# Kernel tuning notes

Hardware: AMD Instinct MI355X
Metric: run time of the kernel (lower is better)

## Reference

```python
import jax, jax.numpy as jnp
import numpy as np

N = 100000      # nodes
E = 640000      # total edges across all relations
D_IN = 128
D_OUT = 128
R = 8           # num_rel
B = 4           # num_bases


def setup_inputs() -> dict:
    key = jax.random.key(0)
    ks = jax.random.split(key, 7)
    return {
        "X": jax.random.normal(ks[0], (N, D_IN), dtype=jnp.float32),
        "edge_src": jax.random.randint(ks[1], (E,), 0, N, dtype=jnp.int32),
        "edge_dst": jax.random.randint(ks[2], (E,), 0, N, dtype=jnp.int32),
        "edge_rel": jax.random.randint(ks[3], (E,), 0, R, dtype=jnp.int32),
        "edge_val": jax.random.uniform(ks[4], (E,), dtype=jnp.float32),
        "w_bases": jax.random.normal(ks[5], (B, D_IN, D_OUT), dtype=jnp.float32) * 0.05,
        "w_rel": jax.random.normal(ks[6], (R, B), dtype=jnp.float32) * 0.5,
    }


def reference(X, edge_src, edge_dst, edge_rel, edge_val, w_bases, w_rel):
    # Per-relation SpMM: support_r = A_r @ X, where A_r rows are destinations.
    # Fuse all relations into one gather + one segmented scatter-add.
    msg = X[edge_src] * edge_val[:, None]                      # [E, D_IN]
    seg = edge_rel.astype(jnp.int32) * N + edge_dst            # combined (rel, dst) id
    supports = jax.ops.segment_sum(msg, seg, num_segments=R * N)
    supports = supports.reshape(R, N, D_IN)                    # == concat of per-rel supports
    # Basis-decomposed relation weights: w[r] = sum_b w_rel[r,b] * w_bases[b]
    w = jnp.einsum("rb,bio->rio", w_rel, w_bases)              # [R, D_IN, D_OUT]
    # cat(supports, dim=1) @ w.view(R*D_IN, D_OUT) == sum_r supports_r @ w_r
    out = jnp.einsum("rni,rio->no", supports, w)               # [N, D_OUT]
    return out
```

## Files before the change

### kernel.cpp

```cpp
#include <hip/hip_runtime.h>
#include <stdint.h>

#define D_IN 128
#define D_OUT 128
#define NREL 8
#define NBASE 4

typedef __attribute__((ext_vector_type(8))) short short8;
typedef __attribute__((ext_vector_type(4))) float floatx4;
typedef __attribute__((ext_vector_type(2))) float floatx2;

__device__ __forceinline__ unsigned short f2bf(float f) {
  unsigned int u = __float_as_uint(f);
  u += 0x7fffu + ((u >> 16) & 1u);
  return (unsigned short)(u >> 16);
}
__device__ __forceinline__ unsigned pack2bf(float lo, float hi) {
  return (unsigned)f2bf(lo) | ((unsigned)f2bf(hi) << 16);
}
__device__ __forceinline__ float bflo(unsigned int u) { return __uint_as_float(u << 16); }
__device__ __forceinline__ float bfhi(unsigned int u) { return __uint_as_float(u & 0xffff0000u); }

__global__ void k_prep(const float4* __restrict__ X, ushort4* __restrict__ Xb, int n4,
                       const float* __restrict__ w_bases, unsigned short* __restrict__ W2T,
                       uint4* __restrict__ counts4, int nc4) {
  int i = blockIdx.x * blockDim.x + threadIdx.x;
  if (i < n4) {
    float4 v = X[i];
    ushort4 o;
    o.x = f2bf(v.x); o.y = f2bf(v.y); o.z = f2bf(v.z); o.w = f2bf(v.w);
    Xb[i] = o;
  }
  if (i < 128 * 512) {
    int o = i >> 9, c = i & 511;
    int k = c >> 2, b = c & 3;
    W2T[i] = f2bf(w_bases[(b * D_IN + k) * D_OUT + o]);
  }
  if (i < nc4) counts4[i] = make_uint4(0u, 0u, 0u, 0u);
}

__global__ void k_count(const int* __restrict__ dst, int* __restrict__ counts, int E) {
  int i = blockIdx.x * blockDim.x + threadIdx.x;
  if (i < E) atomicAdd(&counts[dst[i]], 1);
}

__global__ void k_scan1(const int* __restrict__ counts, int* __restrict__ localsc,
                        int* __restrict__ bsum, int Nn) {
  __shared__ int s[256];
  int i = blockIdx.x * 256 + threadIdx.x;
  int v = (i < Nn) ? counts[i] : 0;
  s[threadIdx.x] = v;
  __syncthreads();
  for (int off = 1; off < 256; off <<= 1) {
    int t = 0;
    if (threadIdx.x >= off) t = s[threadIdx.x - off];
    __syncthreads();
    s[threadIdx.x] += t;
    __syncthreads();
  }
  if (i < Nn) localsc[i] = s[threadIdx.x] - v;
  if (threadIdx.x == 255) bsum[blockIdx.x] = s[255];
}

__global__ void k_scan23(const int* __restrict__ localsc, const int* __restrict__ bsum,
                         int* __restrict__ offsets, int* __restrict__ cursor, int Nn, int E) {
  __shared__ int red[256];
  int acc = 0;
  for (int j = threadIdx.x; j < blockIdx.x; j += 256) acc += bsum[j];
  red[threadIdx.x] = acc;
  __syncthreads();
  for (int off = 128; off > 0; off >>= 1) {
    if (threadIdx.x < off) red[threadIdx.x] += red[threadIdx.x + off];
    __syncthreads();
  }
  int pref = red[0];
  int i = blockIdx.x * 256 + threadIdx.x;
  if (i < Nn) {
    int v = localsc[i] + pref;
    offsets[i] = v;
    cursor[i] = v;
  }
  if (i == 0) offsets[Nn] = E;
}

__global__ void k_bucket(const int* __restrict__ src, const int* __restrict__ dst,
                         const int* __restrict__ rel, const float* __restrict__ val,
                         int* __restrict__ cursor, uint2* __restrict__ bucket, int E) {
  int i = blockIdx.x * blockDim.x + threadIdx.x;
  if (i >= E) return;
  int d = dst[i];
  int pos = atomicAdd(&cursor[d], 1);
  bucket[pos] = make_uint2((unsigned)src[i] | ((unsigned)rel[i] << 21), __float_as_uint(val[i]));
}

__global__ __launch_bounds__(128)
void k_agg_gemm(const uint2* __restrict__ bucket, const int* __restrict__ offsets,
                const float* __restrict__ w_rel_g, const unsigned* __restrict__ Xb2,
                const unsigned short* __restrict__ W2T, float* __restrict__ out, int Nn) {
  __shared__ __align__(16) unsigned short aggS[16][520];
  __shared__ __align__(16) float wrS[NREL * NBASE];
  if (threadIdx.x < NREL * NBASE) wrS[threadIdx.x] = w_rel_g[threadIdx.x];
  __syncthreads();

  const int wave = threadIdx.x >> 6, lane = threadIdx.x & 63;
  const int d0 = blockIdx.x * 16 + wave * 8;
  const unsigned* __restrict__ Xl = Xb2 + lane;
  const floatx2 zf2 = {0.f, 0.f};

  int oidx = d0 + (lane < 8 ? lane : 8);
  if (oidx > Nn) oidx = Nn;
  const int offv = offsets[oidx];
  const int s0 = __builtin_amdgcn_readlane(offv, 0);
  const int e8 = __builtin_amdgcn_readlane(offv, 8);

  floatx2 a0 = zf2, a1 = zf2, a2 = zf2, a3 = zf2;
  int row = 0;
  int bnd = __builtin_amdgcn_readlane(offv, 1);

#define FLUSH()                                                      \
  do {                                                               \
    uint4 o_;                                                        \
    o_.x = pack2bf(a0.x, a1.x);                                      \
    o_.y = pack2bf(a2.x, a3.x);                                      \
    o_.z = pack2bf(a0.y, a1.y);                                      \
    o_.w = pack2bf(a2.y, a3.y);                                      \
    *(uint4*)&aggS[wave * 8 + row][lane * 8] = o_;                   \
    a0 = zf2; a1 = zf2; a2 = zf2; a3 = zf2;                          \
    ++row;                                                           \
    bnd = (row < 8) ? __builtin_amdgcn_readlane(offv, row + 1)       \
                    : 0x7fffffff;                                    \
  } while (0)

#define ACCT(EI, R, V, Y)                                            \
  do {                                                               \
    if ((EI) < e8) {                                                 \
      while ((EI) == bnd) FLUSH();                                   \
      const float4 w_ = *(const float4*)&wrS[((R) >> 21) * 4];       \
      const float val_ = __uint_as_float(V);                         \
      const float c0_ = val_ * w_.x, c1_ = val_ * w_.y;              \
      const float c2_ = val_ * w_.z, c3_ = val_ * w_.w;              \
      floatx2 x_;                                                    \
      x_.x = bflo(Y);                                                \
      x_.y = bfhi(Y);                                                \
      a0 += c0_ * x_;                                                \
      a1 += c1_ * x_;                                                \
      a2 += c2_ * x_;                                                \
      a3 += c3_ * x_;                                                \
    }                                                                \
  } while (0)

#define LOADG(P, BASE)                                               \
  do {                                                               \
    int t0_ = (BASE); if (t0_ > ce) t0_ = ce;                        \
    if (t0_ - cbase >= 64) {                                         \
      cbase += 64;                                                   \
      chC = chN;                                                     \
      int in_ = cbase + 64 + lane;                                   \
      if (in_ > ce) in_ = ce;                                        \
      chN = bucket[in_];                                             \
    }                                                                \
    int t1_ = (BASE) + 1; if (t1_ > ce) t1_ = ce;                    \
    int t2_ = (BASE) + 2; if (t2_ > ce) t2_ = ce;                    \
    int t3_ = (BASE) + 3; if (t3_ > ce) t3_ = ce;                    \
    const int j0_ = t0_ - cbase, j1_ = t1_ - cbase;                  \
    const int j2_ = t2_ - cbase, j3_ = t3_ - cbase;                  \
    r##P##0 = __shfl(chC.x, j0_); v##P##0 = __shfl(chC.y, j0_);      \
    r##P##1 = __shfl(chC.x, j1_); v##P##1 = __shfl(chC.y, j1_);      \
    r##P##2 = __shfl(chC.x, j2_); v##P##2 = __shfl(chC.y, j2_);      \
    r##P##3 = __shfl(chC.x, j3_); v##P##3 = __shfl(chC.y, j3_);      \
    y##P##0 = Xl[(r##P##0 & 0x1FFFFFu) << 6];                        \
    y##P##1 = Xl[(r##P##1 & 0x1FFFFFu) << 6];                        \
    y##P##2 = Xl[(r##P##2 & 0x1FFFFFu) << 6];                        \
    y##P##3 = Xl[(r##P##3 & 0x1FFFFFu) << 6];                        \
  } while (0)

  if (s0 < e8) {
    const int ce = e8 - 1;
    int cbase = s0;
    uint2 chC, chN;
    {
      int i0 = cbase + lane;
      if (i0 > ce) i0 = ce;
      chC = bucket[i0];
      int i1 = cbase + 64 + lane;
      if (i1 > ce) i1 = ce;
      chN = bucket[i1];
    }
    unsigned rA0, rA1, rA2, rA3, vA0, vA1, vA2, vA3, yA0, yA1, yA2, yA3;
    unsigned rB0, rB1, rB2, rB3, vB0, vB1, vB2, vB3, yB0, yB1, yB2, yB3;
    unsigned rC0, rC1, rC2, rC3, vC0, vC1, vC2, vC3, yC0, yC1, yC2, yC3;
    unsigned rD0, rD1, rD2, rD3, vD0, vD1, vD2, vD3, yD0, yD1, yD2, yD3;
    LOADG(A, s0);
    LOADG(B, s0 + 4);
    LOADG(C, s0 + 8);
    int gi = s0;
    while (gi < e8) {
      LOADG(D, gi + 12);
      ACCT(gi, rA0, vA0, yA0);
      ACCT(gi + 1, rA1, vA1, yA1);
      ACCT(gi + 2, rA2, vA2, yA2);
      ACCT(gi + 3, rA3, vA3, yA3);
      LOADG(A, gi + 16);
      ACCT(gi + 4, rB0, vB0, yB0);
      ACCT(gi + 5, rB1, vB1, yB1);
      ACCT(gi + 6, rB2, vB2, yB2);
      ACCT(gi + 7, rB3, vB3, yB3);
      LOADG(B, gi + 20);
      ACCT(gi + 8, rC0, vC0, yC0);
      ACCT(gi + 9, rC1, vC1, yC1);
      ACCT(gi + 10, rC2, vC2, yC2);
      ACCT(gi + 11, rC3, vC3, yC3);
      LOADG(C, gi + 24);
      ACCT(gi + 12, rD0, vD0, yD0);
      ACCT(gi + 13, rD1, vD1, yD1);
      ACCT(gi + 14, rD2, vD2, yD2);
      ACCT(gi + 15, rD3, vD3, yD3);
      gi += 16;
    }
  }
  while (row < 8) FLUSH();

  __syncthreads();

  const int q = lane >> 4, r16 = lane & 15;
  const int wn = wave * 64;
  const floatx4 zero = {0.f, 0.f, 0.f, 0.f};
  floatx4 acc[4];
  acc[0] = zero; acc[1] = zero; acc[2] = zero; acc[3] = zero;

#pragma unroll 4
  for (int k0 = 0; k0 < 512; k0 += 32) {
    int ka = k0 + q * 8;
    short8 af = *(const short8*)&aggS[r16][ka];
    short8 bfv[4];
#pragma unroll
    for (int j = 0; j < 4; ++j)
      bfv[j] = *(const short8*)(W2T + (size_t)(wn + j * 16 + r16) * 512 + ka);
#pragma unroll
    for (int j = 0; j < 4; ++j)
      acc[j] = __builtin_amdgcn_mfma_f32_16x16x32_bf16(af, bfv[j], acc[j], 0, 0, 0);
  }

#pragma unroll
  for (int j = 0; j < 4; ++j) {
#pragma unroll
    for (int p = 0; p < 4; ++p) {
      int prow = q * 4 + p;
      int col = wn + j * 16 + r16;
      int grow = blockIdx.x * 16 + prow;
      if (grow < Nn) out[(size_t)grow * 128 + col] = acc[j][p];
    }
  }
}

extern "C" void kernel_launch(void* const* d_in, const int* in_sizes, int n_in,
                              void* d_out, int out_size, void* d_ws, size_t ws_size,
                              hipStream_t stream) {
  const float* X = (const float*)d_in[0];
  const int* esrc = (const int*)d_in[1];
  const int* edst = (const int*)d_in[2];
  const int* erel = (const int*)d_in[3];
  const float* eval_ = (const float*)d_in[4];
  const float* w_bases = (const float*)d_in[5];
  const float* w_rel = (const float*)d_in[6];
  const int Nn = in_sizes[0] / D_IN;
  const int E = in_sizes[1];

  char* ws = (char*)d_ws;
  size_t off = 0;
  auto alloc = [&](size_t bytes) -> char* {
    char* p = ws + off;
    off += (bytes + 255) & ~(size_t)255;
    return p;
  };
  unsigned short* Xb = (unsigned short*)alloc((size_t)Nn * D_IN * 2);
  unsigned short* W2T = (unsigned short*)alloc((size_t)128 * 512 * 2);
  int* counts = (int*)alloc((size_t)Nn * 4);
  int* cursor = (int*)alloc((size_t)Nn * 4);
  int* offsets = (int*)alloc((size_t)(Nn + 1) * 4);
  int* localsc = (int*)alloc((size_t)Nn * 4);
  int* bsum = (int*)alloc(4096);
  uint2* bucket = (uint2*)alloc((size_t)E * 8);
  (void)ws_size;

  int n4 = Nn * D_IN / 4;
  int nc4 = Nn / 4;
  k_prep<<<(n4 + 255) / 256, 256, 0, stream>>>((const float4*)X, (ushort4*)Xb, n4,
                                               w_bases, W2T, (uint4*)counts, nc4);

  k_count<<<(E + 255) / 256, 256, 0, stream>>>(edst, counts, E);
  int nb = (Nn + 255) / 256;
  k_scan1<<<nb, 256, 0, stream>>>(counts, localsc, bsum, Nn);
  k_scan23<<<nb, 256, 0, stream>>>(localsc, bsum, offsets, cursor, Nn, E);
  k_bucket<<<(E + 255) / 256, 256, 0, stream>>>(esrc, edst, erel, eval_, cursor, bucket, E);

  k_agg_gemm<<<(Nn + 15) / 16, 128, 0, stream>>>(bucket, offsets, w_rel,
                                                 (const unsigned*)Xb, W2T,
                                                 (float*)d_out, Nn);
}
```

Baseline: 290.3 us.

## Fuse edge counting into prep kernel and widen agg-GEMM tile to 32 rows

Edge-destination counting moves into the X/W conversion prep kernel, and a memset replaces the in-kernel counts zeroing, saving one launch. The aggregation+GEMM kernel now uses 256 threads covering 32 destination rows, with each wave computing a 2x2 MFMA tile (32 rows x 32 cols). This halves the W2T loads per output row and raises LDS use per block. The prep kernel grid is sized by n4 (3.2M), which exceeds E, so every edge is still counted.

```diff
diff --git a/kernel.cpp b/kernel.cpp
--- a/kernel.cpp
+++ b/kernel.cpp
@@ -23,7 +23,7 @@
 
 __global__ void k_prep(const float4* __restrict__ X, ushort4* __restrict__ Xb, int n4,
                        const float* __restrict__ w_bases, unsigned short* __restrict__ W2T,
-                       uint4* __restrict__ counts4, int nc4) {
+                       const int* __restrict__ edst, int* __restrict__ counts, int E) {
   int i = blockIdx.x * blockDim.x + threadIdx.x;
   if (i < n4) {
     float4 v = X[i];
@@ -36,12 +36,7 @@
     int k = c >> 2, b = c & 3;
     W2T[i] = f2bf(w_bases[(b * D_IN + k) * D_OUT + o]);
   }
-  if (i < nc4) counts4[i] = make_uint4(0u, 0u, 0u, 0u);
-}
-
-__global__ void k_count(const int* __restrict__ dst, int* __restrict__ counts, int E) {
-  int i = blockIdx.x * blockDim.x + threadIdx.x;
-  if (i < E) atomicAdd(&counts[dst[i]], 1);
+  if (i < E) atomicAdd(&counts[edst[i]], 1);
 }
 
 __global__ void k_scan1(const int* __restrict__ counts, int* __restrict__ localsc,
@@ -93,17 +88,17 @@
   bucket[pos] = make_uint2((unsigned)src[i] | ((unsigned)rel[i] << 21), __float_as_uint(val[i]));
 }
 
-__global__ __launch_bounds__(128)
+__global__ __launch_bounds__(256, 4)
 void k_agg_gemm(const uint2* __restrict__ bucket, const int* __restrict__ offsets,
                 const float* __restrict__ w_rel_g, const unsigned* __restrict__ Xb2,
                 const unsigned short* __restrict__ W2T, float* __restrict__ out, int Nn) {
-  __shared__ __align__(16) unsigned short aggS[16][520];
+  __shared__ __align__(16) unsigned short aggS[32][520];
   __shared__ __align__(16) float wrS[NREL * NBASE];
   if (threadIdx.x < NREL * NBASE) wrS[threadIdx.x] = w_rel_g[threadIdx.x];
   __syncthreads();
 
   const int wave = threadIdx.x >> 6, lane = threadIdx.x & 63;
-  const int d0 = blockIdx.x * 16 + wave * 8;
+  const int d0 = blockIdx.x * 32 + wave * 8;
   const unsigned* __restrict__ Xl = Xb2 + lane;
   const floatx2 zf2 = {0.f, 0.f};
 
@@ -223,32 +218,37 @@
   __syncthreads();
 
   const int q = lane >> 4, r16 = lane & 15;
-  const int wn = wave * 64;
+  const int wn = wave * 32;
   const floatx4 zero = {0.f, 0.f, 0.f, 0.f};
-  floatx4 acc[4];
-  acc[0] = zero; acc[1] = zero; acc[2] = zero; acc[3] = zero;
+  floatx4 acc[2][2];
+  acc[0][0] = zero; acc[0][1] = zero; acc[1][0] = zero; acc[1][1] = zero;
 
 #pragma unroll 4
   for (int k0 = 0; k0 < 512; k0 += 32) {
     int ka = k0 + q * 8;
-    short8 af = *(const short8*)&aggS[r16][ka];
-    short8 bfv[4];
-#pragma unroll
-    for (int j = 0; j < 4; ++j)
-      bfv[j] = *(const short8*)(W2T + (size_t)(wn + j * 16 + r16) * 512 + ka);
-#pragma unroll
-    for (int j = 0; j < 4; ++j)
-      acc[j] = __builtin_amdgcn_mfma_f32_16x16x32_bf16(af, bfv[j], acc[j], 0, 0, 0);
-  }
-
-#pragma unroll
-  for (int j = 0; j < 4; ++j) {
-#pragma unroll
-    for (int p = 0; p < 4; ++p) {
-      int prow = q * 4 + p;
-      int col = wn + j * 16 + r16;
-      int grow = blockIdx.x * 16 + prow;
-      if (grow < Nn) out[(size_t)grow * 128 + col] = acc[j][p];
+    short8 af[2], bfv[2];
+    af[0] = *(const short8*)&aggS[r16][ka];
+    af[1] = *(const short8*)&aggS[16 + r16][ka];
+    bfv[0] = *(const short8*)(W2T + (size_t)(wn + r16) * 512 + ka);
+    bfv[1] = *(const short8*)(W2T + (size_t)(wn + 16 + r16) * 512 + ka);
+#pragma unroll
+    for (int i = 0; i < 2; ++i)
+#pragma unroll
+      for (int j = 0; j < 2; ++j)
+        acc[i][j] = __builtin_amdgcn_mfma_f32_16x16x32_bf16(af[i], bfv[j], acc[i][j], 0, 0, 0);
+  }
+
+#pragma unroll
+  for (int i = 0; i < 2; ++i) {
+#pragma unroll
+    for (int j = 0; j < 2; ++j) {
+#pragma unroll
+      for (int p = 0; p < 4; ++p) {
+        int prow = i * 16 + q * 4 + p;
+        int col = wn + j * 16 + r16;
+        int grow = blockIdx.x * 32 + prow;
+        if (grow < Nn) out[(size_t)grow * 128 + col] = acc[i][j][p];
+      }
     }
   }
 }
@@ -284,17 +284,16 @@
   (void)ws_size;
 
   int n4 = Nn * D_IN / 4;
-  int nc4 = Nn / 4;
+  hipMemsetAsync(counts, 0, (size_t)Nn * 4, stream);
   k_prep<<<(n4 + 255) / 256, 256, 0, stream>>>((const float4*)X, (ushort4*)Xb, n4,
-                                               w_bases, W2T, (uint4*)counts, nc4);
-
-  k_count<<<(E + 255) / 256, 256, 0, stream>>>(edst, counts, E);
+                                               w_bases, W2T, edst, counts, E);
+
   int nb = (Nn + 255) / 256;
   k_scan1<<<nb, 256, 0, stream>>>(counts, localsc, bsum, Nn);
   k_scan23<<<nb, 256, 0, stream>>>(localsc, bsum, offsets, cursor, Nn, E);
   k_bucket<<<(E + 255) / 256, 256, 0, stream>>>(esrc, edst, erel, eval_, cursor, bucket, E);
 
-  k_agg_gemm<<<(Nn + 15) / 16, 128, 0, stream>>>(bucket, offsets, w_rel,
+  k_agg_gemm<<<(Nn + 31) / 32, 256, 0, stream>>>(bucket, offsets, w_rel,
                                                  (const unsigned*)Xb, W2T,
                                                  (float*)d_out, Nn);
 }
```

Measured after the change: 254.9 us. 12.2% less time.
